# Kernel optimization log

Hardware: AMD Instinct MI355X
Metric: run time of the kernel (lower is better)

The kernel has to match this reference:

```python
import jax, jax.numpy as jnp
import numpy as np

C = 512
CQ = C // 8
BN_EPS = 1e-5


def setup_inputs() -> dict:
    key = jax.random.key(0)
    ks = jax.random.split(key, 12)
    s = 0.02
    return {
        "x": jax.random.normal(ks[0], (4, C, 64, 64), dtype=jnp.float32),
        "qw": jax.random.normal(ks[1], (CQ, C), dtype=jnp.float32) * s,
        "qb": jnp.zeros((CQ,), dtype=jnp.float32),
        "kw": jax.random.normal(ks[2], (CQ, C), dtype=jnp.float32) * s,
        "kb": jnp.zeros((CQ,), dtype=jnp.float32),
        "vw": jax.random.normal(ks[3], (C, C), dtype=jnp.float32) * s,
        "vb": jnp.zeros((C,), dtype=jnp.float32),
        "gamma": jnp.zeros((1,), dtype=jnp.float32),
        "beta": jnp.zeros((1,), dtype=jnp.float32),
        "fw": jax.random.normal(ks[4], (C, 2 * C), dtype=jnp.float32) * s,
        "fb": jnp.zeros((C,), dtype=jnp.float32),
        "bn_w": jnp.ones((C,), dtype=jnp.float32),
        "bn_b": jnp.zeros((C,), dtype=jnp.float32),
    }


def reference(x, qw, qb, kw, kb, vw, vb, gamma, beta, fw, fb, bn_w, bn_b):
    b, c, h, w = x.shape
    n = h * w
    xf = x.reshape(b, c, n)  # [b, c, n]

    # ----- position attention -----
    q = jnp.einsum('oc,bcn->bon', qw, xf) + qb[None, :, None]  # [b, cq, n]
    k = jnp.einsum('oc,bcn->bon', kw, xf) + kb[None, :, None]
    v = jnp.einsum('oc,bcn->bon', vw, xf) + vb[None, :, None]  # [b, c, n]
    # scores[i, j] = q_i . k_j, softmax over j
    scores = jnp.einsum('bci,bcj->bij', q, k)  # [b, n, n]
    att = jax.nn.softmax(scores, axis=-1)
    pos = jnp.einsum('bcj,bij->bci', v, att)  # [b, c, n]
    pos_out = (gamma[0] * pos + xf).reshape(b, c, h, w)

    # ----- channel attention -----
    energy = jnp.einsum('bin,bjn->bij', xf, xf)  # [b, c, c]
    catt = jax.nn.softmax(energy, axis=-1)
    chan = jnp.einsum('bij,bjn->bin', catt, xf)
    chan_out = (beta[0] * chan + xf).reshape(b, c, h, w)

    # ----- fusion: 1x1 conv + BN (batch stats, training mode) + ReLU -----
    cat = jnp.concatenate([pos_out, chan_out], axis=1)  # [b, 2c, h, w]
    y = jnp.einsum('oc,bchw->bohw', fw, cat) + fb[None, :, None, None]
    mean = jnp.mean(y, axis=(0, 2, 3), keepdims=True)
    var = jnp.var(y, axis=(0, 2, 3), keepdims=True)
    yn = (y - mean) * jax.lax.rsqrt(var + BN_EPS)
    out = jax.nn.relu(yn * bn_w[None, :, None, None] + bn_b[None, :, None, None])
    return out
```

## Files before the change

kernel.cpp:

```cpp
#include <hip/hip_runtime.h>
#include <stdint.h>

typedef unsigned short u16;
typedef __attribute__((ext_vector_type(8))) short bf16x8;
typedef __attribute__((ext_vector_type(4))) float f32x4;

#define DEVI static __device__ __forceinline__

DEVI u16 f2bf(float f){
  union { float f; uint32_t u; } c; c.f = f;
  uint32_t u = c.u;
  u += 0x7FFFu + ((u >> 16) & 1u);
  return (u16)(u >> 16);
}
DEVI float b2f(u16 h){
  union { uint32_t u; float f; } c; c.u = ((uint32_t)h) << 16;
  return c.f;
}

DEVI void gload16(const u16* g, u16* l){
  __builtin_amdgcn_global_load_lds(
      (const __attribute__((address_space(1))) unsigned int*)g,
      (__attribute__((address_space(3))) unsigned int*)l, 16, 0, 0);
}

DEVI bf16x8 ldsrd(const void* base, int byte){
  return *reinterpret_cast<const bf16x8*>((const char*)base + byte);
}

template<int BM,int BN,int FM,int FN,int BIAS,int EPI,int SWZ,int KSPLIT=1>
__global__ __launch_bounds__(256) void gemm_bt(
    const u16* __restrict__ A, long long strideA, int lda,
    const u16* __restrict__ B, long long strideB, int ldb,
    void* __restrict__ C, long long strideC, int ldc,
    const float* __restrict__ bias, int K,
    const float* __restrict__ cscale, const u16* __restrict__ xadd,
    long long strideX, int ldx)
{
  constexpr int BK  = 32;
  constexpr int WTM = FM*16, WTN = FN*16;
  static_assert(BM == 2*WTM && BN == 2*WTN, "2x2 wave layout");
  __shared__ u16 As[BM*BK];
  __shared__ u16 Bs[BN*BK];

  int bx = blockIdx.x, by = blockIdx.y, bz = blockIdx.z;
  if(SWZ){
    const int gx = gridDim.x, gy = gridDim.y;
    const int nwg = gx * gy * gridDim.z;
    const int orig = bx + gx * (by + gy * bz);
    const int q = nwg >> 3, r = nwg & 7;
    const int xcd = orig & 7, i = orig >> 3;
    const int wg = (xcd < r ? xcd*(q+1) : r*(q+1) + (xcd-r)*q) + i;
    bx = wg % gx;
    const int t = wg / gx;
    by = t % gy;
    bz = t / gy;
  }

  const int zz = bz;
  const int z  = (KSPLIT > 1) ? zz / KSPLIT : zz;
  const int ks = (KSPLIT > 1) ? zz % KSPLIT : 0;
  const u16* Ab = A + (long long)z * strideA + (long long)ks * K;
  const u16* Bb = B + (long long)z * strideB + (long long)ks * K;

  const int tid  = threadIdx.x;
  const int lane = tid & 63, wid = tid >> 6;
  const int wr = wid >> 1, wc = wid & 1;
  const long long bm0 = (long long)by * BM;
  const long long bn0 = (long long)bx * BN;

  const int srow  = lane >> 2;
  const int scol  = (((lane & 3) ^ ((lane >> 3) & 3))) * 8;
  const int wrow  = wid * 16 + srow;
  constexpr int TA = BM/64, TB = BN/64;

  const int fr  = lane & 15;
  const int sl8 = ((lane >> 4) ^ ((lane >> 1) & 3)) * 8;

  f32x4 acc[FM][FN] = {};

  for(int k0 = 0; k0 < K; k0 += BK){
    __syncthreads();
    #pragma unroll
    for(int t=0;t<TA;t++)
      gload16(&Ab[(bm0 + t*64 + wrow)*lda + k0 + scol],
              &As[(t*64 + wid*16)*BK]);
    #pragma unroll
    for(int t=0;t<TB;t++)
      gload16(&Bb[(bn0 + t*64 + wrow)*ldb + k0 + scol],
              &Bs[(t*64 + wid*16)*BK]);
    __syncthreads();

    bf16x8 af[FM], bg[FN];
    #pragma unroll
    for(int m=0;m<FM;m++)
      af[m] = *reinterpret_cast<const bf16x8*>(&As[(wr*WTM + m*16 + fr)*BK + sl8]);
    #pragma unroll
    for(int n=0;n<FN;n++)
      bg[n] = *reinterpret_cast<const bf16x8*>(&Bs[(wc*WTN + n*16 + fr)*BK + sl8]);
    #pragma unroll
    for(int m=0;m<FM;m++)
      #pragma unroll
      for(int n=0;n<FN;n++)
        acc[m][n] = __builtin_amdgcn_mfma_f32_16x16x32_bf16(af[m], bg[n], acc[m][n], 0, 0, 0);
  }

  const int lr = (lane >> 4) * 4, lc = lane & 15;
  const float g = (EPI == 3) ? cscale[0] : 0.f;
  #pragma unroll
  for(int m=0;m<FM;m++){
    #pragma unroll
    for(int n=0;n<FN;n++){
      #pragma unroll
      for(int r=0;r<4;r++){
        long long row = bm0 + wr*WTM + m*16 + lr + r;
        long long col = bn0 + wc*WTN + n*16 + lc;
        float v = acc[m][n][r];
        if(BIAS == 1) v += bias[(int)row];
        if(BIAS == 2) v += bias[(int)col];
        long long idx = row * (long long)ldc + col;
        if(EPI == 0){
          ((float*)C + (long long)zz*strideC)[idx] = v;
        } else if(EPI == 1){
          ((float*)C + (long long)zz*strideC)[idx] += v;
        } else if(EPI == 2){
          ((u16*)C + (long long)zz*strideC)[idx] = f2bf(v);
        } else {
          float xv = b2f(xadd[(long long)z*strideX + row*(long long)ldx + col]);
          ((u16*)C + (long long)zz*strideC)[idx] = f2bf(g * v + xv);
        }
      }
    }
  }
}

__global__ __launch_bounds__(512, 4) void flash_pos(
    const u16* __restrict__ qkT,
    const u16* __restrict__ vB,
    const u16* __restrict__ xfT,
    u16* __restrict__ pcT,
    const float* __restrict__ gamma)
{
  __shared__ u16 Ks[2][64*64];
  __shared__ u16 Vs[256*64];
  __shared__ u16 Ps[64*64];
  __shared__ float RS[2][4][32];

  int flat = blockIdx.x + 64*(blockIdx.y + 2*blockIdx.z);
  flat = (flat & 7)*64 + (flat >> 3);
  const int bx = flat & 63;
  const int ch = (flat >> 6) & 1;
  const int z  = flat >> 7;

  const int q0 = bx*64, c0 = ch*256;
  const int tid = threadIdx.x, lane = tid & 63, wid = tid >> 6;
  const int wr = wid >> 2, wc = wid & 3;
  const int fr = lane & 15, fq = lane >> 4;

  const u16* qkb = qkT + (long long)z*4096*128;
  const u16* vbb = vB  + (long long)z*512*4096;

  const int srow  = lane >> 3;
  const int sslot = (lane & 7) ^ srow;

  bf16x8 qa[2][2];
  #pragma unroll
  for(int m=0;m<2;m++)
    #pragma unroll
    for(int kk=0;kk<2;kk++)
      qa[m][kk] = *reinterpret_cast<const bf16x8*>(
          &qkb[(long long)(q0 + wr*32 + m*16 + fr)*128 + kk*32 + fq*8]);

  const u16* kp  = qkb + (long long)(wid*8 + srow)*128 + 64 + sslot*8;
  const u16* vp0 = vbb + (long long)(c0 + wid*8 + srow)*4096 + sslot*8;

  const int xm   = (fr & 7) << 4;
  const int koff = (wc*16 + fr)*128 + ((fq*16) ^ xm);
  const int pab  = (wr*32 + fr)*128 + ((fq*16) ^ xm);
  const int vfb  = (wc*64 + fr)*128 + ((fq*16) ^ xm);
  const int kdst = wid * 1024;
  const int key2 = (wc*16 + fr)*2;
  int pwo[4];
  #pragma unroll
  for(int r=0;r<4;r++){
    int qr = fq*4 + r;
    pwo[r] = qr*128 + (key2 ^ ((qr & 7) << 4));
  }

  gload16(kp, (u16*)((char*)Ks + kdst));
  kp += 64*128;
  gload16(vp0,            &Vs[(  0 + wid*8)*64]);
  gload16(vp0 +  64*4096, &Vs[( 64 + wid*8)*64]);
  gload16(vp0 + 128*4096, &Vs[(128 + wid*8)*64]);
  gload16(vp0 + 192*4096, &Vs[(192 + wid*8)*64]);
  vp0 += 64;
  __syncthreads();

  f32x4 acc[2][4] = {};
  float rsacc[2][4] = {};

  for(int t=0;t<64;t++){
    const int kbase = (t & 1) ? 8192 : 0;
    bf16x8 kb0 = ldsrd(Ks, kbase + koff);
    bf16x8 kb1 = ldsrd(Ks, kbase + (koff ^ 64));
    f32x4 s[2] = {};
    #pragma unroll
    for(int m=0;m<2;m++){
      s[m] = __builtin_amdgcn_mfma_f32_16x16x32_bf16(qa[m][0], kb0, s[m], 0, 0, 0);
      s[m] = __builtin_amdgcn_mfma_f32_16x16x32_bf16(qa[m][1], kb1, s[m], 0, 0, 0);
    }

    #pragma unroll
    for(int m=0;m<2;m++){
      float e0 = exp2f(s[m][0]), e1 = exp2f(s[m][1]);
      float e2 = exp2f(s[m][2]), e3 = exp2f(s[m][3]);
      rsacc[m][0] += e0; rsacc[m][1] += e1;
      rsacc[m][2] += e2; rsacc[m][3] += e3;
      uint32_t p01, p23;
      asm("v_cvt_pk_bf16_f32 %0, %1, %2" : "=v"(p01) : "v"(e0), "v"(e1));
      asm("v_cvt_pk_bf16_f32 %0, %1, %2" : "=v"(p23) : "v"(e2), "v"(e3));
      char* pbase = (char*)Ps + wr*4096 + m*2048;
      *(u16*)(pbase + pwo[0]) = (u16)p01;
      *(u16*)(pbase + pwo[1]) = (u16)(p01 >> 16);
      *(u16*)(pbase + pwo[2]) = (u16)p23;
      *(u16*)(pbase + pwo[3]) = (u16)(p23 >> 16);
    }
    __syncthreads();

    if(t+1 < 64){
      gload16(kp, (u16*)((char*)Ks + (kbase ^ 8192) + kdst));
      kp += 64*128;
    }

    bf16x8 pa00 = ldsrd(Ps, pab);
    bf16x8 pa01 = ldsrd(Ps, pab ^ 64);
    bf16x8 pa10 = ldsrd(Ps, (pab + 2048));
    bf16x8 pa11 = ldsrd(Ps, (pab + 2048) ^ 64);
    __builtin_amdgcn_s_setprio(1);
    #pragma unroll
    for(int n=0;n<4;n++){
      bf16x8 v0 = ldsrd(Vs, vfb + n*2048);
      bf16x8 v1 = ldsrd(Vs, (vfb + n*2048) ^ 64);
      acc[0][n] = __builtin_amdgcn_mfma_f32_16x16x32_bf16(pa00, v0, acc[0][n], 0, 0, 0);
      acc[0][n] = __builtin_amdgcn_mfma_f32_16x16x32_bf16(pa01, v1, acc[0][n], 0, 0, 0);
      acc[1][n] = __builtin_amdgcn_mfma_f32_16x16x32_bf16(pa10, v0, acc[1][n], 0, 0, 0);
      acc[1][n] = __builtin_amdgcn_mfma_f32_16x16x32_bf16(pa11, v1, acc[1][n], 0, 0, 0);
    }
    __builtin_amdgcn_s_setprio(0);
    __syncthreads();

    if(t+1 < 64){
      gload16(vp0,            &Vs[(  0 + wid*8)*64]);
      gload16(vp0 +  64*4096, &Vs[( 64 + wid*8)*64]);
      gload16(vp0 + 128*4096, &Vs[(128 + wid*8)*64]);
      gload16(vp0 + 192*4096, &Vs[(192 + wid*8)*64]);
      vp0 += 64;
    }
  }

  #pragma unroll
  for(int m=0;m<2;m++)
    #pragma unroll
    for(int r=0;r<4;r++){
      float v = rsacc[m][r];
      #pragma unroll
      for(int o=1;o<16;o<<=1) v += __shfl_xor(v, o);
      rsacc[m][r] = v;
    }
  if(fr == 0){
    #pragma unroll
    for(int m=0;m<2;m++)
      #pragma unroll
      for(int r=0;r<4;r++)
        RS[wr][wc][m*16 + fq*4 + r] = rsacc[m][r];
  }
  __syncthreads();

  const float g = gamma[0];
  #pragma unroll
  for(int m=0;m<2;m++){
    float inv[4];
    #pragma unroll
    for(int r=0;r<4;r++){
      int rloc = m*16 + fq*4 + r;
      inv[r] = g / (RS[wr][0][rloc] + RS[wr][1][rloc] +
                    RS[wr][2][rloc] + RS[wr][3][rloc]);
    }
    #pragma unroll
    for(int n=0;n<4;n++){
      #pragma unroll
      for(int r=0;r<4;r++){
        int qrow = q0 + wr*32 + m*16 + fq*4 + r;
        int c    = c0 + wc*64 + n*16 + fr;
        float xv = b2f(xfT[((long long)z*4096 + qrow)*512 + c]);
        pcT[((long long)z*4096 + qrow)*1024 + c] = f2bf(acc[m][n][r]*inv[r] + xv);
      }
    }
  }
}

__global__ __launch_bounds__(256) void softmax_sum4(const u16* __restrict__ part,
                                                    u16* __restrict__ catt)
{
  const int row = blockIdx.x;
  const int b = row >> 9, i = row & 511;
  const int t = threadIdx.x;
  const int lane = t & 63, wid = t >> 6;
  float v0 = 0.f, v1 = 0.f;
  #pragma unroll
  for(int sl=0;sl<4;sl++){
    uint32_t pr = *reinterpret_cast<const uint32_t*>(
        &part[(((long long)(b*4 + sl)*512 + i)*512) + 2*t]);
    v0 += b2f((u16)pr);
    v1 += b2f((u16)(pr >> 16));
  }
  float m = fmaxf(v0, v1);
  #pragma unroll
  for(int o=32;o;o>>=1) m = fmaxf(m, __shfl_xor(m, o));
  __shared__ float sred[4];
  if(lane == 0) sred[wid] = m;
  __syncthreads();
  m = fmaxf(fmaxf(sred[0], sred[1]), fmaxf(sred[2], sred[3]));
  float e0 = __expf(v0 - m), e1 = __expf(v1 - m);
  float s = e0 + e1;
  #pragma unroll
  for(int o=32;o;o>>=1) s += __shfl_xor(s, o);
  __syncthreads();
  if(lane == 0) sred[wid] = s;
  __syncthreads();
  s = sred[0] + sred[1] + sred[2] + sred[3];
  float inv = 1.0f / s;
  uint32_t pk = (uint32_t)f2bf(e0 * inv) | ((uint32_t)f2bf(e1 * inv) << 16);
  *reinterpret_cast<uint32_t*>(&catt[(long long)row * 512 + 2*t]) = pk;
}

__global__ __launch_bounds__(256) void prep_weights(
    const float* __restrict__ qw, const float* __restrict__ kw,
    const float* __restrict__ vw, const float* __restrict__ fw,
    const float* __restrict__ qb, const float* __restrict__ kb,
    u16* __restrict__ qkwb, u16* __restrict__ vwb, u16* __restrict__ fwb,
    float* __restrict__ qkb)
{
  const float LOG2E = 1.4426950408889634f;
  long long i = (long long)blockIdx.x*256 + threadIdx.x;
  const float* src; u16* dst; long long o; float sc = 1.f;
  if(i < 8192){        src = qw; dst = qkwb;          o = i; sc = LOG2E; }
  else if(i < 16384){  src = kw; dst = qkwb + 32768;  o = i - 8192; }
  else if(i < 81920){  src = vw; dst = vwb;           o = i - 16384; }
  else if(i < 212992){ src = fw; dst = fwb;           o = i - 81920; }
  else if(i < 213024){
    int t = (int)(i - 212992) * 4;
    #pragma unroll
    for(int j=0;j<4;j++) qkb[t+j] = (t+j < 64) ? qb[t+j]*LOG2E : kb[t+j-64];
    return;
  } else return;
  float4 v = reinterpret_cast<const float4*>(src)[o];
  ushort4 w;
  w.x = f2bf(v.x*sc); w.y = f2bf(v.y*sc); w.z = f2bf(v.z*sc); w.w = f2bf(v.w*sc);
  reinterpret_cast<ushort4*>(dst)[o] = w;
}

__global__ __launch_bounds__(256) void transpose_cast(
    const float* __restrict__ x, u16* __restrict__ xfb, u16* __restrict__ xfT)
{
  __shared__ float tile[32][33];
  const int b  = blockIdx.z;
  const int n0 = blockIdx.x * 32, c0 = blockIdx.y * 32;
  const int tx = threadIdx.x, ty = threadIdx.y;
  const float* xp = x + (long long)b * 512 * 4096;
  #pragma unroll
  for(int i=0;i<4;i++){
    int c = c0 + ty + i*8;
    float v = xp[(long long)c*4096 + n0 + tx];
    tile[ty + i*8][tx] = v;
    xfb[((long long)b*512 + c)*4096 + n0 + tx] = f2bf(v);
  }
  __syncthreads();
  #pragma unroll
  for(int i=0;i<4;i++){
    int n = n0 + ty + i*8;
    xfT[((long long)b*4096 + n)*512 + c0 + tx] = f2bf(tile[tx][ty + i*8]);
  }
}

__global__ __launch_bounds__(256) void bn_stats(const float* __restrict__ y,
                                                float* __restrict__ stat)
{
  const int o = blockIdx.x, t = threadIdx.x;
  const int lane = t & 63, wid = t >> 6;
  float s = 0.f, ss = 0.f;
  for(int b=0;b<4;b++){
    const float* p = y + ((long long)b*512 + o)*4096;
    for(int i=t;i<4096;i+=256){ float v = p[i]; s += v; ss += v*v; }
  }
  #pragma unroll
  for(int off=32;off;off>>=1){ s += __shfl_xor(s, off); ss += __shfl_xor(ss, off); }
  __shared__ float sred[8];
  if(lane == 0){ sred[wid] = s; sred[wid+4] = ss; }
  __syncthreads();
  if(t == 0){
    float S  = sred[0]+sred[1]+sred[2]+sred[3];
    float SS = sred[4]+sred[5]+sred[6]+sred[7];
    float mean = S * (1.f/16384.f);
    float var  = SS * (1.f/16384.f) - mean*mean;
    stat[o*2]   = mean;
    stat[o*2+1] = rsqrtf(var + 1e-5f);
  }
}

__global__ __launch_bounds__(256) void bn_apply(float* __restrict__ y,
    const float* __restrict__ stat, const float* __restrict__ w,
    const float* __restrict__ bb)
{
  long long i = (long long)blockIdx.x*256 + threadIdx.x;
  float4 v = reinterpret_cast<float4*>(y)[i];
  int o = (int)(((i*4) >> 12) & 511);
  float mean = stat[o*2], rstd = stat[o*2+1];
  float sc = w[o] * rstd;
  float sh = bb[o] - mean * sc;
  v.x = fmaxf(v.x*sc + sh, 0.f);
  v.y = fmaxf(v.y*sc + sh, 0.f);
  v.z = fmaxf(v.z*sc + sh, 0.f);
  v.w = fmaxf(v.w*sc + sh, 0.f);
  reinterpret_cast<float4*>(y)[i] = v;
}

extern "C" void kernel_launch(void* const* d_in, const int* in_sizes, int n_in,
                              void* d_out, int out_size, void* d_ws, size_t ws_size,
                              hipStream_t stream)
{
  const float* x     = (const float*)d_in[0];
  const float* qw    = (const float*)d_in[1];
  const float* qb    = (const float*)d_in[2];
  const float* kw    = (const float*)d_in[3];
  const float* kb    = (const float*)d_in[4];
  const float* vw    = (const float*)d_in[5];
  const float* vb    = (const float*)d_in[6];
  const float* gamma = (const float*)d_in[7];
  const float* beta  = (const float*)d_in[8];
  const float* fw    = (const float*)d_in[9];
  const float* fb    = (const float*)d_in[10];
  const float* bnw   = (const float*)d_in[11];
  const float* bnb   = (const float*)d_in[12];
  float* out = (float*)d_out;
  (void)in_sizes; (void)n_in; (void)out_size; (void)ws_size;

  char* base = (char*)d_ws;
  size_t off = 0;
  auto alloc = [&](size_t bytes)->char* {
    char* p = base + off;
    off += (bytes + 255) & ~(size_t)255;
    return p;
  };
  const long long NB = 4, Cc = 512, Nn = 4096;

  u16*   xfT  = (u16*)alloc((size_t)NB*Nn*Cc*2);
  u16*   xfb  = (u16*)alloc((size_t)NB*Cc*Nn*2);
  u16*   qkwb = (u16*)alloc((size_t)128*Cc*2);
  float* qkb  = (float*)alloc(128*4);
  u16*   vwb  = (u16*)alloc((size_t)Cc*Cc*2);
  u16*   fwb  = (u16*)alloc((size_t)Cc*2*Cc*2);
  u16*   qkT  = (u16*)alloc((size_t)NB*Nn*128*2);
  u16*   vB   = (u16*)alloc((size_t)NB*Cc*Nn*2);
  u16*   pcT  = (u16*)alloc((size_t)NB*Nn*1024*2);
  u16*   epart= (u16*)alloc((size_t)16*Cc*Cc*2);
  u16*   catt = (u16*)alloc((size_t)NB*Cc*Cc*2);
  float* stat = (float*)alloc((size_t)Cc*2*4);

  prep_weights<<<dim3(833), dim3(256), 0, stream>>>(qw, kw, vw, fw, qb, kb,
                                                    qkwb, vwb, fwb, qkb);
  transpose_cast<<<dim3(128,16,4), dim3(32,8), 0, stream>>>(x, xfb, xfT);

  gemm_bt<64,64,2,2,2,2,1><<<dim3(2,64,4), dim3(256), 0, stream>>>(
      xfT, Nn*Cc, 512, qkwb, 0, 512, qkT, Nn*128, 128, qkb, 512,
      nullptr, nullptr, 0, 0);
  gemm_bt<128,128,4,4,1,2,1><<<dim3(32,4,4), dim3(256), 0, stream>>>(
      vwb, 0, 512, xfT, Nn*Cc, 512, vB, Cc*Nn, 4096, vb, 512,
      nullptr, nullptr, 0, 0);

  gemm_bt<128,128,4,4,0,2,1,4><<<dim3(4,4,16), dim3(256), 0, stream>>>(
      xfb, Cc*Nn, 4096, xfb, Cc*Nn, 4096, epart, Cc*Cc, 512, nullptr, 1024,
      nullptr, nullptr, 0, 0);
  softmax_sum4<<<dim3(2048), dim3(256), 0, stream>>>(epart, catt);
  gemm_bt<128,128,4,4,0,3,1><<<dim3(4,32,4), dim3(256), 0, stream>>>(
      xfT, Nn*Cc, 512, catt, Cc*Cc, 512, pcT + 512, Nn*1024, 1024, nullptr, 512,
      beta, xfT, Nn*Cc, 512);

  flash_pos<<<dim3(64,2,4), dim3(512), 0, stream>>>(qkT, vB, xfT, pcT, gamma);

  gemm_bt<128,128,4,4,1,0,1><<<dim3(32,4,4), dim3(256), 0, stream>>>(
      fwb, 0, 1024, pcT, Nn*1024, 1024, out, Cc*Nn, 4096, fb, 1024,
      nullptr, nullptr, 0, 0);

  bn_stats<<<dim3(512), dim3(256), 0, stream>>>(out, stat);
  bn_apply<<<dim3(8192), dim3(256), 0, stream>>>(out, stat, bnw, bnb);
}
```

Before: 260.4 us.

## Fold fusion conv weights into value and channel-attention matrices, fuse BN stats

Uses linearity to fold the fusion 1x1 conv weights into the value projection (fw·vw) and into the channel-attention matrix (fw2·catt plus fw1+fw2 for the residual). The final GEMM then runs over K=512 instead of 1024, and the large pcT concat buffer and the channel-attention output GEMM are removed. The final GEMM epilogue adds the flash output, writes bf16 and emits per-column BN partial sums, which replaces the separate full-tensor stats pass. A transposed BN apply then writes the fp32 output. In exchange it adds small weight-prep GEMMs and extra kernels, and moves more work into bf16 (the y intermediate and the combined weights), which risks accuracy.

```diff
diff --git a/kernel.cpp b/kernel.cpp
--- a/kernel.cpp
+++ b/kernel.cpp
@@ -35,7 +35,7 @@
     void* __restrict__ C, long long strideC, int ldc,
     const float* __restrict__ bias, int K,
     const float* __restrict__ cscale, const u16* __restrict__ xadd,
-    long long strideX, int ldx)
+    long long strideX, int ldx, float* __restrict__ red)
 {
   constexpr int BK  = 32;
   constexpr int WTM = FM*16, WTN = FN*16;
@@ -106,6 +106,36 @@
   }
 
   const int lr = (lane >> 4) * 4, lc = lane & 15;
+
+  if(EPI == 8){
+    u16* Cp = (u16*)C + (long long)zz*strideC;
+    #pragma unroll
+    for(int n=0;n<FN;n++){
+      long long col = bn0 + wc*WTN + n*16 + lc;
+      float bv = bias[(int)col];
+      float s = 0.f, ss = 0.f;
+      #pragma unroll
+      for(int m=0;m<FM;m++){
+        #pragma unroll
+        for(int r=0;r<4;r++){
+          long long row = bm0 + wr*WTM + m*16 + lr + r;
+          long long idx = row*(long long)ldc + col;
+          float v = acc[m][n][r] + bv + b2f(Cp[idx]);
+          Cp[idx] = f2bf(v);
+          s += v; ss += v*v;
+        }
+      }
+      s += __shfl_xor(s,16); ss += __shfl_xor(ss,16);
+      s += __shfl_xor(s,32); ss += __shfl_xor(ss,32);
+      if(lane < 16){
+        int slot = (z*(int)gridDim.y + by)*2 + wr;
+        red[col*512 + slot*2]     = s;
+        red[col*512 + slot*2 + 1] = ss;
+      }
+    }
+    return;
+  }
+
   const float g = (EPI == 3) ? cscale[0] : 0.f;
   #pragma unroll
   for(int m=0;m<FM;m++){
@@ -137,8 +167,7 @@
 __global__ __launch_bounds__(512, 4) void flash_pos(
     const u16* __restrict__ qkT,
     const u16* __restrict__ vB,
-    const u16* __restrict__ xfT,
-    u16* __restrict__ pcT,
+    u16* __restrict__ yT,
     const float* __restrict__ gamma)
 {
   __shared__ u16 Ks[2][64*64];
@@ -216,14 +245,11 @@
       float e2 = exp2f(s[m][2]), e3 = exp2f(s[m][3]);
       rsacc[m][0] += e0; rsacc[m][1] += e1;
       rsacc[m][2] += e2; rsacc[m][3] += e3;
-      uint32_t p01, p23;
-      asm("v_cvt_pk_bf16_f32 %0, %1, %2" : "=v"(p01) : "v"(e0), "v"(e1));
-      asm("v_cvt_pk_bf16_f32 %0, %1, %2" : "=v"(p23) : "v"(e2), "v"(e3));
       char* pbase = (char*)Ps + wr*4096 + m*2048;
-      *(u16*)(pbase + pwo[0]) = (u16)p01;
-      *(u16*)(pbase + pwo[1]) = (u16)(p01 >> 16);
-      *(u16*)(pbase + pwo[2]) = (u16)p23;
-      *(u16*)(pbase + pwo[3]) = (u16)(p23 >> 16);
+      *(u16*)(pbase + pwo[0]) = f2bf(e0);
+      *(u16*)(pbase + pwo[1]) = f2bf(e1);
+      *(u16*)(pbase + pwo[2]) = f2bf(e2);
+      *(u16*)(pbase + pwo[3]) = f2bf(e3);
     }
     __syncthreads();
 
@@ -277,6 +303,7 @@
   __syncthreads();
 
   const float g = gamma[0];
+  u16* yb = yT + (long long)z*4096*512;
   #pragma unroll
   for(int m=0;m<2;m++){
     float inv[4];
@@ -292,15 +319,14 @@
       for(int r=0;r<4;r++){
         int qrow = q0 + wr*32 + m*16 + fq*4 + r;
         int c    = c0 + wc*64 + n*16 + fr;
-        float xv = b2f(xfT[((long long)z*4096 + qrow)*512 + c]);
-        pcT[((long long)z*4096 + qrow)*1024 + c] = f2bf(acc[m][n][r]*inv[r] + xv);
+        yb[(long long)qrow*512 + c] = f2bf(acc[m][n][r]*inv[r]);
       }
     }
   }
 }
 
-__global__ __launch_bounds__(256) void softmax_sum4(const u16* __restrict__ part,
-                                                    u16* __restrict__ catt)
+__global__ __launch_bounds__(256) void esum_stats(const u16* __restrict__ part,
+                                                  float* __restrict__ st)
 {
   const int row = blockIdx.x;
   const int b = row >> 9, i = row & 511;
@@ -321,43 +347,95 @@
   if(lane == 0) sred[wid] = m;
   __syncthreads();
   m = fmaxf(fmaxf(sred[0], sred[1]), fmaxf(sred[2], sred[3]));
-  float e0 = __expf(v0 - m), e1 = __expf(v1 - m);
-  float s = e0 + e1;
+  float s = __expf(v0 - m) + __expf(v1 - m);
   #pragma unroll
   for(int o=32;o;o>>=1) s += __shfl_xor(s, o);
   __syncthreads();
   if(lane == 0) sred[wid] = s;
   __syncthreads();
-  s = sred[0] + sred[1] + sred[2] + sred[3];
-  float inv = 1.0f / s;
-  uint32_t pk = (uint32_t)f2bf(e0 * inv) | ((uint32_t)f2bf(e1 * inv) << 16);
-  *reinterpret_cast<uint32_t*>(&catt[(long long)row * 512 + 2*t]) = pk;
+  if(t == 0){
+    st[row*2]   = m;
+    st[row*2+1] = sred[0] + sred[1] + sred[2] + sred[3];
+  }
+}
+
+__global__ __launch_bounds__(256) void catt_apply(const u16* __restrict__ part,
+                                                  const float* __restrict__ st,
+                                                  u16* __restrict__ cattT)
+{
+  const int row = blockIdx.x;
+  const int b = row >> 9, i = row & 511;
+  const int t = threadIdx.x;
+  float v0 = 0.f, v1 = 0.f;
+  #pragma unroll
+  for(int sl=0;sl<4;sl++){
+    uint32_t pr = *reinterpret_cast<const uint32_t*>(
+        &part[(((long long)(b*4 + sl)*512 + i)*512) + 2*t]);
+    v0 += b2f((u16)pr);
+    v1 += b2f((u16)(pr >> 16));
+  }
+  float4 ms = reinterpret_cast<const float4*>(st)[b*256 + t];
+  float o0 = __expf(v0 - ms.x) / ms.y;
+  float o1 = __expf(v1 - ms.z) / ms.w;
+  uint32_t pk = (uint32_t)f2bf(o0) | ((uint32_t)f2bf(o1) << 16);
+  *reinterpret_cast<uint32_t*>(&cattT[(long long)row * 512 + 2*t]) = pk;
 }
 
 __global__ __launch_bounds__(256) void prep_weights(
     const float* __restrict__ qw, const float* __restrict__ kw,
     const float* __restrict__ vw, const float* __restrict__ fw,
     const float* __restrict__ qb, const float* __restrict__ kb,
-    u16* __restrict__ qkwb, u16* __restrict__ vwb, u16* __restrict__ fwb,
-    float* __restrict__ qkb)
+    u16* __restrict__ qkwb, u16* __restrict__ vwT, u16* __restrict__ fwb,
+    u16* __restrict__ fw12, float* __restrict__ qkb)
 {
   const float LOG2E = 1.4426950408889634f;
   long long i = (long long)blockIdx.x*256 + threadIdx.x;
-  const float* src; u16* dst; long long o; float sc = 1.f;
-  if(i < 8192){        src = qw; dst = qkwb;          o = i; sc = LOG2E; }
-  else if(i < 16384){  src = kw; dst = qkwb + 32768;  o = i - 8192; }
-  else if(i < 81920){  src = vw; dst = vwb;           o = i - 16384; }
-  else if(i < 212992){ src = fw; dst = fwb;           o = i - 81920; }
-  else if(i < 213024){
+  if(i < 8192){
+    float4 v = reinterpret_cast<const float4*>(qw)[i];
+    ushort4 w = { f2bf(v.x*LOG2E), f2bf(v.y*LOG2E), f2bf(v.z*LOG2E), f2bf(v.w*LOG2E) };
+    reinterpret_cast<ushort4*>(qkwb)[i] = w;
+  } else if(i < 16384){
+    long long o = i - 8192;
+    float4 v = reinterpret_cast<const float4*>(kw)[o];
+    ushort4 w = { f2bf(v.x), f2bf(v.y), f2bf(v.z), f2bf(v.w) };
+    reinterpret_cast<ushort4*>(qkwb + 32768)[o] = w;
+  } else if(i < 81920){
+    long long o = i - 16384;
+    float4 v = reinterpret_cast<const float4*>(vw)[o];
+    int c  = (int)(o >> 7);
+    int cp = (int)(o & 127) * 4;
+    vwT[(cp+0)*512 + c] = f2bf(v.x);
+    vwT[(cp+1)*512 + c] = f2bf(v.y);
+    vwT[(cp+2)*512 + c] = f2bf(v.z);
+    vwT[(cp+3)*512 + c] = f2bf(v.w);
+  } else if(i < 212992){
+    long long o = i - 81920;
+    float4 v = reinterpret_cast<const float4*>(fw)[o];
+    ushort4 w = { f2bf(v.x), f2bf(v.y), f2bf(v.z), f2bf(v.w) };
+    reinterpret_cast<ushort4*>(fwb)[o] = w;
+    int row = (int)(o >> 8);
+    int c4  = (int)(o & 255) * 4;
+    if(c4 < 512){
+      float4 v2 = reinterpret_cast<const float4*>(fw)[o + 128];
+      ushort4 s = { f2bf(v.x+v2.x), f2bf(v.y+v2.y), f2bf(v.z+v2.z), f2bf(v.w+v2.w) };
+      reinterpret_cast<ushort4*>(fw12)[row*128 + (c4>>2)] = s;
+    }
+  } else if(i < 213024){
     int t = (int)(i - 212992) * 4;
     #pragma unroll
     for(int j=0;j<4;j++) qkb[t+j] = (t+j < 64) ? qb[t+j]*LOG2E : kb[t+j-64];
-    return;
-  } else return;
-  float4 v = reinterpret_cast<const float4*>(src)[o];
-  ushort4 w;
-  w.x = f2bf(v.x*sc); w.y = f2bf(v.y*sc); w.z = f2bf(v.z*sc); w.w = f2bf(v.w*sc);
-  reinterpret_cast<ushort4*>(dst)[o] = w;
+  }
+}
+
+__global__ __launch_bounds__(256) void fwvb(const float* __restrict__ fw,
+                                            const float* __restrict__ vb,
+                                            float* __restrict__ bp)
+{
+  int o = blockIdx.x*256 + threadIdx.x;
+  if(o >= 512) return;
+  float s = 0.f;
+  for(int c=0;c<512;c++) s += fw[o*1024 + c] * vb[c];
+  bp[o] = s;
 }
 
 __global__ __launch_bounds__(256) void transpose_cast(
@@ -383,46 +461,45 @@
   }
 }
 
-__global__ __launch_bounds__(256) void bn_stats(const float* __restrict__ y,
-                                                float* __restrict__ stat)
-{
-  const int o = blockIdx.x, t = threadIdx.x;
-  const int lane = t & 63, wid = t >> 6;
+__global__ __launch_bounds__(256) void bn_finalize(const float* __restrict__ red,
+                                                   float* __restrict__ stat)
+{
+  int ch = blockIdx.x*256 + threadIdx.x;
+  if(ch >= 512) return;
   float s = 0.f, ss = 0.f;
-  for(int b=0;b<4;b++){
-    const float* p = y + ((long long)b*512 + o)*4096;
-    for(int i=t;i<4096;i+=256){ float v = p[i]; s += v; ss += v*v; }
-  }
-  #pragma unroll
-  for(int off=32;off;off>>=1){ s += __shfl_xor(s, off); ss += __shfl_xor(ss, off); }
-  __shared__ float sred[8];
-  if(lane == 0){ sred[wid] = s; sred[wid+4] = ss; }
-  __syncthreads();
-  if(t == 0){
-    float S  = sred[0]+sred[1]+sred[2]+sred[3];
-    float SS = sred[4]+sred[5]+sred[6]+sred[7];
-    float mean = S * (1.f/16384.f);
-    float var  = SS * (1.f/16384.f) - mean*mean;
-    stat[o*2]   = mean;
-    stat[o*2+1] = rsqrtf(var + 1e-5f);
-  }
-}
-
-__global__ __launch_bounds__(256) void bn_apply(float* __restrict__ y,
+  for(int j=0;j<256;j++){
+    s  += red[ch*512 + j*2];
+    ss += red[ch*512 + j*2 + 1];
+  }
+  float mean = s * (1.f/16384.f);
+  float var  = ss * (1.f/16384.f) - mean*mean;
+  stat[ch*2]   = mean;
+  stat[ch*2+1] = rsqrtf(var + 1e-5f);
+}
+
+__global__ __launch_bounds__(256) void bn_apply_t(const u16* __restrict__ yT,
     const float* __restrict__ stat, const float* __restrict__ w,
-    const float* __restrict__ bb)
-{
-  long long i = (long long)blockIdx.x*256 + threadIdx.x;
-  float4 v = reinterpret_cast<float4*>(y)[i];
-  int o = (int)(((i*4) >> 12) & 511);
-  float mean = stat[o*2], rstd = stat[o*2+1];
-  float sc = w[o] * rstd;
-  float sh = bb[o] - mean * sc;
-  v.x = fmaxf(v.x*sc + sh, 0.f);
-  v.y = fmaxf(v.y*sc + sh, 0.f);
-  v.z = fmaxf(v.z*sc + sh, 0.f);
-  v.w = fmaxf(v.w*sc + sh, 0.f);
-  reinterpret_cast<float4*>(y)[i] = v;
+    const float* __restrict__ bb, float* __restrict__ out)
+{
+  __shared__ float tile[32][33];
+  const int b  = blockIdx.z;
+  const int n0 = blockIdx.x * 32, c0 = blockIdx.y * 32;
+  const int tx = threadIdx.x, ty = threadIdx.y;
+  const int ch = c0 + tx;
+  const float sc = w[ch] * stat[ch*2+1];
+  const float sh = bb[ch] - stat[ch*2] * sc;
+  #pragma unroll
+  for(int i=0;i<4;i++){
+    int n = n0 + ty + i*8;
+    float v = b2f(yT[((long long)b*4096 + n)*512 + ch]);
+    tile[ty + i*8][tx] = fmaxf(v*sc + sh, 0.f);
+  }
+  __syncthreads();
+  #pragma unroll
+  for(int i=0;i<4;i++){
+    int c = c0 + ty + i*8;
+    out[((long long)b*512 + c)*4096 + n0 + tx] = tile[tx][ty + i*8];
+  }
 }
 
 extern "C" void kernel_launch(void* const* d_in, const int* in_sizes, int n_in,
@@ -456,42 +533,55 @@
 
   u16*   xfT  = (u16*)alloc((size_t)NB*Nn*Cc*2);
   u16*   xfb  = (u16*)alloc((size_t)NB*Cc*Nn*2);
+  u16*   fwb  = (u16*)alloc((size_t)Cc*2*Cc*2);
   u16*   qkwb = (u16*)alloc((size_t)128*Cc*2);
   float* qkb  = (float*)alloc(128*4);
-  u16*   vwb  = (u16*)alloc((size_t)Cc*Cc*2);
-  u16*   fwb  = (u16*)alloc((size_t)Cc*2*Cc*2);
+  u16*   vwT  = (u16*)alloc((size_t)Cc*Cc*2);
+  u16*   Wp   = (u16*)alloc((size_t)Cc*Cc*2);
+  u16*   fw12 = (u16*)alloc((size_t)Cc*Cc*2);
+  float* bp   = (float*)alloc(Cc*4);
   u16*   qkT  = (u16*)alloc((size_t)NB*Nn*128*2);
   u16*   vB   = (u16*)alloc((size_t)NB*Cc*Nn*2);
-  u16*   pcT  = (u16*)alloc((size_t)NB*Nn*1024*2);
   u16*   epart= (u16*)alloc((size_t)16*Cc*Cc*2);
-  u16*   catt = (u16*)alloc((size_t)NB*Cc*Cc*2);
+  u16*   cattT= (u16*)alloc((size_t)NB*Cc*Cc*2);
+  u16*   Mb   = (u16*)alloc((size_t)NB*Cc*Cc*2);
+  float* st2  = (float*)alloc((size_t)NB*Cc*2*4);
   float* stat = (float*)alloc((size_t)Cc*2*4);
+  float* red  = (float*)alloc((size_t)Cc*256*2*4);
+  u16*   yT   = xfb;
 
   prep_weights<<<dim3(833), dim3(256), 0, stream>>>(qw, kw, vw, fw, qb, kb,
-                                                    qkwb, vwb, fwb, qkb);
+                                                    qkwb, vwT, fwb, fw12, qkb);
+  fwvb<<<dim3(2), dim3(256), 0, stream>>>(fw, vb, bp);
   transpose_cast<<<dim3(128,16,4), dim3(32,8), 0, stream>>>(x, xfb, xfT);
 
-  gemm_bt<64,64,2,2,2,2,1><<<dim3(2,64,4), dim3(256), 0, stream>>>(
+  gemm_bt<64,64,2,2,0,2,1><<<dim3(8,8,1), dim3(256), 0, stream>>>(
+      fwb, 0, 1024, vwT, 0, 512, Wp, 0, 512, nullptr, 512,
+      nullptr, nullptr, 0, 0, nullptr);
+
+  gemm_bt<64,128,2,4,2,2,1><<<dim3(1,64,4), dim3(256), 0, stream>>>(
       xfT, Nn*Cc, 512, qkwb, 0, 512, qkT, Nn*128, 128, qkb, 512,
-      nullptr, nullptr, 0, 0);
+      nullptr, nullptr, 0, 0, nullptr);
   gemm_bt<128,128,4,4,1,2,1><<<dim3(32,4,4), dim3(256), 0, stream>>>(
-      vwb, 0, 512, xfT, Nn*Cc, 512, vB, Cc*Nn, 4096, vb, 512,
-      nullptr, nullptr, 0, 0);
+      Wp, 0, 512, xfT, Nn*Cc, 512, vB, Cc*Nn, 4096, bp, 512,
+      nullptr, nullptr, 0, 0, nullptr);
 
   gemm_bt<128,128,4,4,0,2,1,4><<<dim3(4,4,16), dim3(256), 0, stream>>>(
       xfb, Cc*Nn, 4096, xfb, Cc*Nn, 4096, epart, Cc*Cc, 512, nullptr, 1024,
-      nullptr, nullptr, 0, 0);
-  softmax_sum4<<<dim3(2048), dim3(256), 0, stream>>>(epart, catt);
-  gemm_bt<128,128,4,4,0,3,1><<<dim3(4,32,4), dim3(256), 0, stream>>>(
-      xfT, Nn*Cc, 512, catt, Cc*Cc, 512, pcT + 512, Nn*1024, 1024, nullptr, 512,
-      beta, xfT, Nn*Cc, 512);
-
-  flash_pos<<<dim3(64,2,4), dim3(512), 0, stream>>>(qkT, vB, xfT, pcT, gamma);
-
-  gemm_bt<128,128,4,4,1,0,1><<<dim3(32,4,4), dim3(256), 0, stream>>>(
-      fwb, 0, 1024, pcT, Nn*1024, 1024, out, Cc*Nn, 4096, fb, 1024,
-      nullptr, nullptr, 0, 0);
-
-  bn_stats<<<dim3(512), dim3(256), 0, stream>>>(out, stat);
-  bn_apply<<<dim3(8192), dim3(256), 0, stream>>>(out, stat, bnw, bnb);
-}
+      nullptr, nullptr, 0, 0, nullptr);
+  esum_stats<<<dim3(2048), dim3(256), 0, stream>>>(epart, st2);
+  catt_apply<<<dim3(2048), dim3(256), 0, stream>>>(epart, st2, cattT);
+
+  gemm_bt<64,64,2,2,0,3,1><<<dim3(8,8,4), dim3(256), 0, stream>>>(
+      fwb + 512, 0, 1024, cattT, Cc*Cc, 512, Mb, Cc*Cc, 512, nullptr, 512,
+      beta, fw12, 0, 512, nullptr);
+
+  flash_pos<<<dim3(64,2,4), dim3(512), 0, stream>>>(qkT, vB, yT, gamma);
+
+  gemm_bt<128,128,4,4,2,8,1><<<dim3(4,32,4), dim3(256), 0, stream>>>(
+      xfT, Nn*Cc, 512, Mb, Cc*Cc, 512, yT, Nn*Cc, 512, fb, 512,
+      nullptr, nullptr, 0, 0, red);
+
+  bn_finalize<<<dim3(2), dim3(256), 0, stream>>>(red, stat);
+  bn_apply_t<<<dim3(128,16,4), dim3(32,8), 0, stream>>>(yT, stat, bnw, bnb, out);
+}
```

New measurement: 275.8 us. +5.9%, slower.
